# Kernel optimization log

Measured on AMD Instinct MI355X. Metric: run time of the kernel, lower is better.

Reference implementation:

```python
import jax, jax.numpy as jnp
import numpy as np

DIM = 1024
RANK = 8
POOL = 16
SCALE = 8.0 / 8.0  # alpha / rank


def setup_inputs() -> dict:
    key = jax.random.key(0)
    ks = jax.random.split(key, 8)
    B, N = 8, 4096
    x = jax.random.normal(ks[0], (B, N, DIM), dtype=jnp.float32)
    weight = jax.random.normal(ks[1], (3 * DIM, DIM), dtype=jnp.float32) * 0.02
    bias = jax.random.normal(ks[2], (3 * DIM,), dtype=jnp.float32) * 0.02
    A_q_pool = jax.random.normal(ks[3], (POOL, DIM, RANK), dtype=jnp.float32) * 0.02
    B_q_pool = jax.random.normal(ks[4], (POOL, RANK, DIM), dtype=jnp.float32) * 0.02
    A_v_pool = jax.random.normal(ks[5], (POOL, DIM, RANK), dtype=jnp.float32) * 0.02
    B_v_pool = jax.random.normal(ks[6], (POOL, RANK, DIM), dtype=jnp.float32) * 0.02
    idx = jax.random.randint(ks[7], (B, 1), 0, POOL, dtype=jnp.int64 if jax.config.jax_enable_x64 else jnp.int32)
    frozen_mask = jnp.zeros((POOL,), dtype=bool)
    return {"x": x, "weight": weight, "bias": bias,
            "A_q_pool": A_q_pool, "B_q_pool": B_q_pool,
            "A_v_pool": A_v_pool, "B_v_pool": B_v_pool,
            "idx": idx, "frozen_mask": frozen_mask}


def _maybe_freeze(pool, i, fz):
    g = pool[i]  # [B, ., .] per-sample gather
    return jnp.where(fz, jax.lax.stop_gradient(g), g)


def reference(x, weight, bias, A_q_pool, B_q_pool, A_v_pool, B_v_pool, idx, frozen_mask):
    # Base QKV projection: [B, N, 3*dim]
    qkv = jnp.einsum('bni,oi->bno', x, weight) + bias
    i = idx[:, 0]                      # [B]
    fz = frozen_mask[i][:, None, None]  # [B,1,1]
    A_q = _maybe_freeze(A_q_pool, i, fz)  # [B, dim, rank]
    B_q = _maybe_freeze(B_q_pool, i, fz)  # [B, rank, dim]
    A_v = _maybe_freeze(A_v_pool, i, fz)
    B_v = _maybe_freeze(B_v_pool, i, fz)
    # Low-rank update: (x @ A) @ B, rank-8 bottleneck
    new_q = jnp.einsum('bnr,brj->bnj', jnp.einsum('bni,bir->bnr', x, A_q), B_q)
    new_v = jnp.einsum('bnr,brj->bnj', jnp.einsum('bni,bir->bnr', x, A_v), B_v)
    qkv = qkv.at[:, :, :DIM].add(SCALE * new_q)
    qkv = qkv.at[:, :, -DIM:].add(SCALE * new_v)
    return qkv
```

## Files before the change

### kernel.cpp

```cpp
#include <hip/hip_runtime.h>
#include <hip/hip_bf16.h>
#include <stdint.h>

#define DIM   1024
#define ODIM  3072
#define MROWS 32768
#define RANK  8

typedef unsigned short u16;
typedef __attribute__((ext_vector_type(8))) short short8;
typedef __attribute__((ext_vector_type(8))) unsigned short u16x8;
typedef __attribute__((ext_vector_type(4))) unsigned short u16x4;
typedef __attribute__((ext_vector_type(4))) float f32x4;

__device__ __forceinline__ u16 f2bf(float f) {
    uint32_t u = __float_as_uint(f);
    u += 0x7fffu + ((u >> 16) & 1u);
    return (u16)(u >> 16);
}

__device__ __forceinline__ void gl2lds16(const void* g, void* l) {
    __builtin_amdgcn_global_load_lds(
        (const __attribute__((address_space(1))) void*)(uintptr_t)g,
        (__attribute__((address_space(3))) void*)(uint32_t)(uintptr_t)l,
        16, 0, 0);
}

#define BAR()    do { asm volatile("" ::: "memory"); __builtin_amdgcn_s_barrier(); asm volatile("" ::: "memory"); } while (0)
#define WAITV10() asm volatile("s_waitcnt vmcnt(10)" ::: "memory")
#define WAITV8()  asm volatile("s_waitcnt vmcnt(8)" ::: "memory")
#define WAITV4()  asm volatile("s_waitcnt vmcnt(4)" ::: "memory")
#define WAITV2()  asm volatile("s_waitcnt vmcnt(2)" ::: "memory")
#define WAITV0()  asm volatile("s_waitcnt vmcnt(0)" ::: "memory")
#define SCHED0()  __builtin_amdgcn_sched_barrier(0)

__global__ __launch_bounds__(256) void k_convert(const float* __restrict__ src,
                                                 u16* __restrict__ dst, int n) {
    const int stride = gridDim.x * blockDim.x;
    for (int t = blockIdx.x * blockDim.x + threadIdx.x; t * 8 < n; t += stride) {
        const int i = t * 8;
        float4 a = *reinterpret_cast<const float4*>(src + i);
        float4 b = *reinterpret_cast<const float4*>(src + i + 4);
        u16x8 o;
        o[0] = f2bf(a.x); o[1] = f2bf(a.y); o[2] = f2bf(a.z); o[3] = f2bf(a.w);
        o[4] = f2bf(b.x); o[5] = f2bf(b.y); o[6] = f2bf(b.z); o[7] = f2bf(b.w);
        *reinterpret_cast<u16x8*>(dst + i) = o;
    }
}

__global__ __launch_bounds__(256) void k_build(const float* __restrict__ W,
                                               const float* __restrict__ Aq_pool,
                                               const float* __restrict__ Bq_pool,
                                               const float* __restrict__ Av_pool,
                                               const float* __restrict__ Bv_pool,
                                               const int* __restrict__ idx,
                                               u16* __restrict__ Wmq,
                                               u16* __restrict__ Wmv) {
    const int b  = blockIdx.x >> 7;
    const int s  = (blockIdx.x >> 6) & 1;
    const int og = blockIdx.x & 63;
    const int p  = idx[b];
    const float* A  = (s ? Av_pool : Aq_pool) + (size_t)p * DIM * RANK;
    const float* Bp = (s ? Bv_pool : Bq_pool) + (size_t)p * RANK * DIM;
    const float* Ws = W + (size_t)(s ? 2048 : 0) * DIM;
    u16* dst = (s ? Wmv : Wmq) + (size_t)b * DIM * DIM;

    const int t  = threadIdx.x;
    const int i0 = t * 4;
    float a[4][8];
    #pragma unroll
    for (int ii = 0; ii < 4; ++ii) {
        float4 a0 = reinterpret_cast<const float4*>(A + (size_t)(i0 + ii) * RANK)[0];
        float4 a1 = reinterpret_cast<const float4*>(A + (size_t)(i0 + ii) * RANK)[1];
        a[ii][0] = a0.x; a[ii][1] = a0.y; a[ii][2] = a0.z; a[ii][3] = a0.w;
        a[ii][4] = a1.x; a[ii][5] = a1.y; a[ii][6] = a1.z; a[ii][7] = a1.w;
    }
    for (int r = 0; r < 16; ++r) {
        const int o = og * 16 + r;
        float bv[8];
        #pragma unroll
        for (int rr = 0; rr < 8; ++rr) bv[rr] = Bp[(size_t)rr * DIM + o];
        float4 w = *reinterpret_cast<const float4*>(Ws + (size_t)o * DIM + i0);
        float v[4] = {w.x, w.y, w.z, w.w};
        u16x4 ov;
        #pragma unroll
        for (int ii = 0; ii < 4; ++ii) {
            float d = 0.f;
            #pragma unroll
            for (int rr = 0; rr < 8; ++rr) d += a[ii][rr] * bv[rr];
            ov[ii] = f2bf(v[ii] + d);
        }
        *reinterpret_cast<u16x4*>(dst + (size_t)o * DIM + i0) = ov;
    }
}


__device__ __forceinline__ void stage_half(const u16* __restrict__ mat, int row0, int tk,
                                           u16* dst, int wave, int lane) {
    const int lrow = lane >> 3;
    const int g    = (lane & 7) ^ lrow;
    const u16* gp = mat + (size_t)(row0 + wave * 8 + lrow) * DIM + tk + g * 8;
    u16* lp = dst + wave * 8 * 64;
    gl2lds16(gp, lp);
    gl2lds16(gp + (size_t)64 * DIM, lp + 64 * 64);
}

__device__ __forceinline__ void ds_read_A(const u16* sA, int wr, int lane,
                                          int kx0, int kx1, int mh, short8 (&a)[4][2]) {
    #pragma unroll
    for (int f = 0; f < 4; ++f) {
        const int row = wr * 64 + f * 16 + mh * 128 + (lane & 15);
        a[f][0] = *reinterpret_cast<const short8*>(sA + row * 64 + kx0);
        a[f][1] = *reinterpret_cast<const short8*>(sA + row * 64 + kx1);
    }
}
__device__ __forceinline__ void ds_read_B(const u16* sB, int wc, int lane,
                                          int kx0, int kx1, int nh, short8 (&b)[2][2]) {
    #pragma unroll
    for (int f = 0; f < 2; ++f) {
        const int row = wc * 16 + (nh * 2 + f) * 64 + (lane & 15);
        b[f][0] = *reinterpret_cast<const short8*>(sB + row * 64 + kx0);
        b[f][1] = *reinterpret_cast<const short8*>(sB + row * 64 + kx1);
    }
}

template <int MH, int NH>
__device__ __forceinline__ void mfma_quad(const short8 (&a)[4][2], const short8 (&b)[2][2],
                                          f32x4 (&acc)[8][4]) {
    #pragma unroll
    for (int ks = 0; ks < 2; ++ks)
        #pragma unroll
        for (int f = 0; f < 4; ++f)
            #pragma unroll
            for (int g = 0; g < 2; ++g)
                acc[MH * 4 + f][NH * 2 + g] = __builtin_amdgcn_mfma_f32_16x16x32_bf16(
                    a[f][ks], b[g][ks], acc[MH * 4 + f][NH * 2 + g], 0, 0, 0);
}

#define PHASE(MH, NH, BREG)                             \
    do {                                                \
        BAR();                                          \
        SCHED0();                                       \
        __builtin_amdgcn_s_setprio(1);                  \
        mfma_quad<MH, NH>(a, BREG, acc);                \
        __builtin_amdgcn_s_setprio(0);                  \
        SCHED0();                                       \
    } while (0)

__global__ __launch_bounds__(512, 2) void k_gemm(const u16* __restrict__ Xc,
                                                 const u16* __restrict__ Wk,
                                                 const u16* __restrict__ Wmq,
                                                 const u16* __restrict__ Wmv,
                                                 const float* __restrict__ bias,
                                                 float* __restrict__ out) {
    extern __shared__ u16 lds[];
    const int tid  = threadIdx.x;
    const int lane = tid & 63, wave = tid >> 6;
    const int wr = wave >> 2, wc = wave & 3;

    const int orig = blockIdx.x;
    const int wg   = (orig & 7) * 192 + (orig >> 3);
    const int bn   = wg % 12;
    const int bm   = wg / 12;
    const int m0 = bm * 256, n0 = bn * 256;
    const int batch = m0 >> 12;

    const u16* Bmat;
    int nc;
    if (n0 < DIM)           { Bmat = Wmq + (size_t)batch * DIM * DIM; nc = n0; }
    else if (n0 < 2 * DIM)  { Bmat = Wk;                              nc = n0 - DIM; }
    else                    { Bmat = Wmv + (size_t)batch * DIM * DIM; nc = n0 - 2 * DIM; }

    const int kx0 = (((lane >> 4)    ) ^ (lane & 7)) * 8;
    const int kx1 = (((lane >> 4) + 4) ^ (lane & 7)) * 8;

    f32x4 acc[8][4] = {};

    stage_half(Xc,   m0,       0, lds,                    wave, lane);
    stage_half(Bmat, nc,       0, lds + 16384,            wave, lane);
    stage_half(Bmat, nc + 128, 0, lds + 16384 + 128 * 64, wave, lane);
    stage_half(Xc,   m0 + 128, 0, lds + 128 * 64,         wave, lane);
    WAITV0(); BAR();

    #pragma unroll 1
    for (int t = 0; t < 15; ++t) {
        const u16* sA = lds + (t & 1) * 32768;
        const u16* sB = sA + 16384;
        u16* wA = lds + ((t + 1) & 1) * 32768;
        u16* wB = wA + 16384;
        const int tk1 = (t + 1) * 64;
        short8 a[4][2], b0[2][2], b1[2][2];

        ds_read_A(sA, wr, lane, kx0, kx1, 0, a);
        ds_read_B(sB, wc, lane, kx0, kx1, 0, b0);
        stage_half(Xc,   m0,       tk1, wA,            wave, lane);
        stage_half(Bmat, nc,       tk1, wB,            wave, lane);
        stage_half(Bmat, nc + 128, tk1, wB + 128 * 64, wave, lane);
        stage_half(Xc,   m0 + 128, tk1, wA + 128 * 64, wave, lane);
        PHASE(0, 0, b0);
        WAITV10(); BAR();

        ds_read_B(sB, wc, lane, kx0, kx1, 1, b1);
        PHASE(0, 1, b1);
        WAITV8(); BAR();

        ds_read_A(sA, wr, lane, kx0, kx1, 1, a);
        PHASE(1, 0, b0);
        BAR();

        PHASE(1, 1, b1);
        WAITV4(); BAR();
    }

    {
        const u16* sA = lds + 32768;
        const u16* sB = sA + 16384;
        short8 a[4][2], b0[2][2], b1[2][2];

        ds_read_A(sA, wr, lane, kx0, kx1, 0, a);
        ds_read_B(sB, wc, lane, kx0, kx1, 0, b0);
        PHASE(0, 0, b0);
        WAITV2(); BAR();

        ds_read_B(sB, wc, lane, kx0, kx1, 1, b1);
        PHASE(0, 1, b1);
        WAITV0(); BAR();

        ds_read_A(sA, wr, lane, kx0, kx1, 1, a);
        PHASE(1, 0, b0);
        BAR();

        PHASE(1, 1, b1);
    }

    const int cn = wc * 16 + (lane & 15);
    float bcol[4];
    #pragma unroll
    for (int ni = 0; ni < 4; ++ni) bcol[ni] = bias[n0 + cn + ni * 64];
    #pragma unroll
    for (int mi = 0; mi < 8; ++mi) {
        const int rb = m0 + wr * 64 + (mi & 3) * 16 + (mi >> 2) * 128 + (lane >> 4) * 4;
        #pragma unroll
        for (int v = 0; v < 4; ++v) {
            const size_t row = (size_t)(rb + v);
            #pragma unroll
            for (int ni = 0; ni < 4; ++ni)
                out[row * ODIM + (size_t)(n0 + cn + ni * 64)] = acc[mi][ni][v] + bcol[ni];
        }
    }
}

extern "C" void kernel_launch(void* const* d_in, const int* in_sizes, int n_in,
                              void* d_out, int out_size, void* d_ws, size_t ws_size,
                              hipStream_t stream) {
    const float* x      = (const float*)d_in[0];
    const float* weight = (const float*)d_in[1];
    const float* bias   = (const float*)d_in[2];
    const float* Aq     = (const float*)d_in[3];
    const float* Bq     = (const float*)d_in[4];
    const float* Av     = (const float*)d_in[5];
    const float* Bv     = (const float*)d_in[6];
    const int*   idx    = (const int*)d_in[7];
    float* out = (float*)d_out;

    u16* Xc  = (u16*)d_ws;
    u16* Wk  = Xc + (size_t)MROWS * DIM;
    u16* Wmq = Wk + (size_t)DIM * DIM;
    u16* Wmv = Wmq + (size_t)8 * DIM * DIM;

    hipFuncSetAttribute(reinterpret_cast<const void*>(k_gemm),
                        hipFuncAttributeMaxDynamicSharedMemorySize, 131072);

    k_convert<<<2048, 256, 0, stream>>>(x, Xc, MROWS * DIM);
    k_convert<<<512, 256, 0, stream>>>(weight + (size_t)DIM * DIM, Wk, DIM * DIM);
    k_build<<<1024, 256, 0, stream>>>(weight, Aq, Bq, Av, Bv, idx, Wmq, Wmv);
    k_gemm<<<1536, 512, 131072, stream>>>(Xc, Wk, Wmq, Wmv, bias, out);
}
```

Measured before the change: 330.6 us.

## Restructure GEMM to 16 waves with triple-buffered BK=32 LDS pipeline

Rewrites the main GEMM mainloop to use 1024-thread blocks (16 waves, each owning a 64x64 sub-tile), K-step 32 instead of 64, and a three-stage LDS ring buffer that keeps two loads in flight. The goal is to hide global-to-LDS latency better and simplify the phase-by-phase barrier schedule. Per-wave accumulator count halves, which lowers register pressure. The costs are more barriers per unit of K, thinner MFMA bursts between syncs, and 96KB of LDS per block, which caps occupancy. The idx argument is added but unused.

Measured after the change: 324.9 us. Within noise of the previous version (-1.7%).

```diff
diff --git a/kernel.cpp b/kernel.cpp
--- a/kernel.cpp
+++ b/kernel.cpp
@@ -6,6 +6,7 @@
 #define ODIM  3072
 #define MROWS 32768
 #define RANK  8
+#define BK    32
 
 typedef unsigned short u16;
 typedef __attribute__((ext_vector_type(8))) short short8;
@@ -27,12 +28,8 @@
 }
 
 #define BAR()    do { asm volatile("" ::: "memory"); __builtin_amdgcn_s_barrier(); asm volatile("" ::: "memory"); } while (0)
-#define WAITV10() asm volatile("s_waitcnt vmcnt(10)" ::: "memory")
-#define WAITV8()  asm volatile("s_waitcnt vmcnt(8)" ::: "memory")
-#define WAITV4()  asm volatile("s_waitcnt vmcnt(4)" ::: "memory")
-#define WAITV2()  asm volatile("s_waitcnt vmcnt(2)" ::: "memory")
-#define WAITV0()  asm volatile("s_waitcnt vmcnt(0)" ::: "memory")
-#define SCHED0()  __builtin_amdgcn_sched_barrier(0)
+#define WAITV2() asm volatile("s_waitcnt vmcnt(2)" ::: "memory")
+#define WAITV0() asm volatile("s_waitcnt vmcnt(0)" ::: "memory")
 
 __global__ __launch_bounds__(256) void k_convert(const float* __restrict__ src,
                                                  u16* __restrict__ dst, int n) {
@@ -95,64 +92,44 @@
 }
 
 
-__device__ __forceinline__ void stage_half(const u16* __restrict__ mat, int row0, int tk,
-                                           u16* dst, int wave, int lane) {
-    const int lrow = lane >> 3;
-    const int g    = (lane & 7) ^ lrow;
-    const u16* gp = mat + (size_t)(row0 + wave * 8 + lrow) * DIM + tk + g * 8;
-    u16* lp = dst + wave * 8 * 64;
-    gl2lds16(gp, lp);
-    gl2lds16(gp + (size_t)64 * DIM, lp + 64 * 64);
-}
-
-__device__ __forceinline__ void ds_read_A(const u16* sA, int wr, int lane,
-                                          int kx0, int kx1, int mh, short8 (&a)[4][2]) {
-    #pragma unroll
-    for (int f = 0; f < 4; ++f) {
-        const int row = wr * 64 + f * 16 + mh * 128 + (lane & 15);
-        a[f][0] = *reinterpret_cast<const short8*>(sA + row * 64 + kx0);
-        a[f][1] = *reinterpret_cast<const short8*>(sA + row * 64 + kx1);
-    }
-}
-__device__ __forceinline__ void ds_read_B(const u16* sB, int wc, int lane,
-                                          int kx0, int kx1, int nh, short8 (&b)[2][2]) {
-    #pragma unroll
-    for (int f = 0; f < 2; ++f) {
-        const int row = wc * 16 + (nh * 2 + f) * 64 + (lane & 15);
-        b[f][0] = *reinterpret_cast<const short8*>(sB + row * 64 + kx0);
-        b[f][1] = *reinterpret_cast<const short8*>(sB + row * 64 + kx1);
-    }
-}
-
-template <int MH, int NH>
-__device__ __forceinline__ void mfma_quad(const short8 (&a)[4][2], const short8 (&b)[2][2],
-                                          f32x4 (&acc)[8][4]) {
-    #pragma unroll
-    for (int ks = 0; ks < 2; ++ks)
-        #pragma unroll
-        for (int f = 0; f < 4; ++f)
-            #pragma unroll
-            for (int g = 0; g < 2; ++g)
-                acc[MH * 4 + f][NH * 2 + g] = __builtin_amdgcn_mfma_f32_16x16x32_bf16(
-                    a[f][ks], b[g][ks], acc[MH * 4 + f][NH * 2 + g], 0, 0, 0);
-}
-
-#define PHASE(MH, NH, BREG)                             \
-    do {                                                \
-        BAR();                                          \
-        SCHED0();                                       \
-        __builtin_amdgcn_s_setprio(1);                  \
-        mfma_quad<MH, NH>(a, BREG, acc);                \
-        __builtin_amdgcn_s_setprio(0);                  \
-        SCHED0();                                       \
-    } while (0)
-
-__global__ __launch_bounds__(512, 2) void k_gemm(const u16* __restrict__ Xc,
-                                                 const u16* __restrict__ Wk,
-                                                 const u16* __restrict__ Wmq,
-                                                 const u16* __restrict__ Wmv,
-                                                 const float* __restrict__ bias,
-                                                 float* __restrict__ out) {
+__device__ __forceinline__ void stage(const u16* __restrict__ Xc,
+                                      const u16* __restrict__ Bm,
+                                      int m0, int nc, int tk,
+                                      u16* buf, int wave, int lane) {
+    const int rl = lane >> 2;
+    const int gs = (lane & 3) ^ ((lane >> 2) & 3) ^ ((lane >> 4) & 3);
+    const u16* ga = Xc + (size_t)(m0 + wave * 16 + rl) * DIM + tk + gs * 8;
+    const u16* gb = Bm + (size_t)(nc + wave * 16 + rl) * DIM + tk + gs * 8;
+    gl2lds16(ga, buf + wave * 512);
+    gl2lds16(gb, buf + 8192 + wave * 512);
+}
+
+__device__ __forceinline__ void tile_mfma(const u16* __restrict__ buf,
+                                          int wr, int wc, int lane, int kx,
+                                          f32x4 (&acc)[4][4]) {
+    short8 a[4], b[4];
+    #pragma unroll
+    for (int f = 0; f < 4; ++f)
+        a[f] = *reinterpret_cast<const short8*>(buf + (wr * 64 + f * 16 + (lane & 15)) * 32 + kx);
+    #pragma unroll
+    for (int n = 0; n < 4; ++n)
+        b[n] = *reinterpret_cast<const short8*>(buf + 8192 + (wc * 64 + n * 16 + (lane & 15)) * 32 + kx);
+    __builtin_amdgcn_s_setprio(1);
+    #pragma unroll
+    for (int f = 0; f < 4; ++f)
+        #pragma unroll
+        for (int n = 0; n < 4; ++n)
+            acc[f][n] = __builtin_amdgcn_mfma_f32_16x16x32_bf16(a[f], b[n], acc[f][n], 0, 0, 0);
+    __builtin_amdgcn_s_setprio(0);
+}
+
+__global__ __launch_bounds__(1024, 4) void k_gemm(const u16* __restrict__ Xc,
+                                                  const u16* __restrict__ Wk,
+                                                  const u16* __restrict__ Wmq,
+                                                  const u16* __restrict__ Wmv,
+                                                  const float* __restrict__ bias,
+                                                  const int* __restrict__ idx,
+                                                  float* __restrict__ out) {
     extern __shared__ u16 lds[];
     const int tid  = threadIdx.x;
     const int lane = tid & 63, wave = tid >> 6;
@@ -171,81 +148,49 @@
     else if (n0 < 2 * DIM)  { Bmat = Wk;                              nc = n0 - DIM; }
     else                    { Bmat = Wmv + (size_t)batch * DIM * DIM; nc = n0 - 2 * DIM; }
 
-    const int kx0 = (((lane >> 4)    ) ^ (lane & 7)) * 8;
-    const int kx1 = (((lane >> 4) + 4) ^ (lane & 7)) * 8;
-
-    f32x4 acc[8][4] = {};
-
-    stage_half(Xc,   m0,       0, lds,                    wave, lane);
-    stage_half(Bmat, nc,       0, lds + 16384,            wave, lane);
-    stage_half(Bmat, nc + 128, 0, lds + 16384 + 128 * 64, wave, lane);
-    stage_half(Xc,   m0 + 128, 0, lds + 128 * 64,         wave, lane);
+    const int kx = ((lane >> 4) ^ (lane & 3) ^ ((lane >> 2) & 3)) * 8;
+
+    u16* b0 = lds;
+    u16* b1 = lds + 16384;
+    u16* b2 = lds + 32768;
+
+    f32x4 acc[4][4] = {};
+
+    stage(Xc, Bmat, m0, nc, 0,  b0, wave, lane);
+    stage(Xc, Bmat, m0, nc, BK, b1, wave, lane);
+    WAITV2(); BAR();
+
+    #pragma unroll 1
+    for (int t3 = 0; t3 < 30; t3 += 3) {
+        stage(Xc, Bmat, m0, nc, (t3 + 2) * BK, b2, wave, lane);
+        tile_mfma(b0, wr, wc, lane, kx, acc);
+        WAITV2(); BAR();
+
+        stage(Xc, Bmat, m0, nc, (t3 + 3) * BK, b0, wave, lane);
+        tile_mfma(b1, wr, wc, lane, kx, acc);
+        WAITV2(); BAR();
+
+        stage(Xc, Bmat, m0, nc, (t3 + 4) * BK, b1, wave, lane);
+        tile_mfma(b2, wr, wc, lane, kx, acc);
+        WAITV2(); BAR();
+    }
+    tile_mfma(b0, wr, wc, lane, kx, acc);
     WAITV0(); BAR();
-
-    #pragma unroll 1
-    for (int t = 0; t < 15; ++t) {
-        const u16* sA = lds + (t & 1) * 32768;
-        const u16* sB = sA + 16384;
-        u16* wA = lds + ((t + 1) & 1) * 32768;
-        u16* wB = wA + 16384;
-        const int tk1 = (t + 1) * 64;
-        short8 a[4][2], b0[2][2], b1[2][2];
-
-        ds_read_A(sA, wr, lane, kx0, kx1, 0, a);
-        ds_read_B(sB, wc, lane, kx0, kx1, 0, b0);
-        stage_half(Xc,   m0,       tk1, wA,            wave, lane);
-        stage_half(Bmat, nc,       tk1, wB,            wave, lane);
-        stage_half(Bmat, nc + 128, tk1, wB + 128 * 64, wave, lane);
-        stage_half(Xc,   m0 + 128, tk1, wA + 128 * 64, wave, lane);
-        PHASE(0, 0, b0);
-        WAITV10(); BAR();
-
-        ds_read_B(sB, wc, lane, kx0, kx1, 1, b1);
-        PHASE(0, 1, b1);
-        WAITV8(); BAR();
-
-        ds_read_A(sA, wr, lane, kx0, kx1, 1, a);
-        PHASE(1, 0, b0);
-        BAR();
-
-        PHASE(1, 1, b1);
-        WAITV4(); BAR();
-    }
-
-    {
-        const u16* sA = lds + 32768;
-        const u16* sB = sA + 16384;
-        short8 a[4][2], b0[2][2], b1[2][2];
-
-        ds_read_A(sA, wr, lane, kx0, kx1, 0, a);
-        ds_read_B(sB, wc, lane, kx0, kx1, 0, b0);
-        PHASE(0, 0, b0);
-        WAITV2(); BAR();
-
-        ds_read_B(sB, wc, lane, kx0, kx1, 1, b1);
-        PHASE(0, 1, b1);
-        WAITV0(); BAR();
-
-        ds_read_A(sA, wr, lane, kx0, kx1, 1, a);
-        PHASE(1, 0, b0);
-        BAR();
-
-        PHASE(1, 1, b1);
-    }
-
-    const int cn = wc * 16 + (lane & 15);
+    tile_mfma(b1, wr, wc, lane, kx, acc);
+
+    const int cn = wc * 64 + (lane & 15);
     float bcol[4];
     #pragma unroll
-    for (int ni = 0; ni < 4; ++ni) bcol[ni] = bias[n0 + cn + ni * 64];
-    #pragma unroll
-    for (int mi = 0; mi < 8; ++mi) {
-        const int rb = m0 + wr * 64 + (mi & 3) * 16 + (mi >> 2) * 128 + (lane >> 4) * 4;
+    for (int n = 0; n < 4; ++n) bcol[n] = bias[n0 + cn + n * 16];
+    #pragma unroll
+    for (int f = 0; f < 4; ++f) {
+        const int rb = m0 + wr * 64 + f * 16 + (lane >> 4) * 4;
         #pragma unroll
         for (int v = 0; v < 4; ++v) {
             const size_t row = (size_t)(rb + v);
             #pragma unroll
-            for (int ni = 0; ni < 4; ++ni)
-                out[row * ODIM + (size_t)(n0 + cn + ni * 64)] = acc[mi][ni][v] + bcol[ni];
+            for (int n = 0; n < 4; ++n)
+                out[row * ODIM + (size_t)(n0 + cn + n * 16)] = acc[f][n][v] + bcol[n];
         }
     }
 }
@@ -269,10 +214,10 @@
     u16* Wmv = Wmq + (size_t)8 * DIM * DIM;
 
     hipFuncSetAttribute(reinterpret_cast<const void*>(k_gemm),
-                        hipFuncAttributeMaxDynamicSharedMemorySize, 131072);
+                        hipFuncAttributeMaxDynamicSharedMemorySize, 98304);
 
     k_convert<<<2048, 256, 0, stream>>>(x, Xc, MROWS * DIM);
     k_convert<<<512, 256, 0, stream>>>(weight + (size_t)DIM * DIM, Wk, DIM * DIM);
     k_build<<<1024, 256, 0, stream>>>(weight, Aq, Bq, Av, Bv, idx, Wmq, Wmv);
-    k_gemm<<<1536, 512, 131072, stream>>>(Xc, Wk, Wmq, Wmv, bias, out);
-}
+    k_gemm<<<1536, 1024, 98304, stream>>>(Xc, Wk, Wmq, Wmv, bias, idx, out);
+}
```

## Interleave global-to-LDS staging across MFMA phases and split A fragment registers

Applied to the files above, without the earlier changes.

Spreads the four global-to-LDS stage_half loads of the next K tile across the four MFMA phases instead of issuing them all up front. Separate A register sets are used for the low and high M halves, and explicit lgkmcnt waits are added before each MFMA block. The vmcnt thresholds are retuned to match the new issue order. This is meant to smooth memory issue and overlap it with MFMA work, at the cost of more VGPRs and possibly tighter sync stalls.

Result: faster. 298.2 us (-9.8%).

```diff
diff --git a/kernel.cpp b/kernel.cpp
--- a/kernel.cpp
+++ b/kernel.cpp
@@ -27,12 +27,12 @@
 }
 
 #define BAR()    do { asm volatile("" ::: "memory"); __builtin_amdgcn_s_barrier(); asm volatile("" ::: "memory"); } while (0)
-#define WAITV10() asm volatile("s_waitcnt vmcnt(10)" ::: "memory")
-#define WAITV8()  asm volatile("s_waitcnt vmcnt(8)" ::: "memory")
-#define WAITV4()  asm volatile("s_waitcnt vmcnt(4)" ::: "memory")
-#define WAITV2()  asm volatile("s_waitcnt vmcnt(2)" ::: "memory")
-#define WAITV0()  asm volatile("s_waitcnt vmcnt(0)" ::: "memory")
-#define SCHED0()  __builtin_amdgcn_sched_barrier(0)
+#define WAITV4() asm volatile("s_waitcnt vmcnt(4)" ::: "memory")
+#define WAITV2() asm volatile("s_waitcnt vmcnt(2)" ::: "memory")
+#define WAITV0() asm volatile("s_waitcnt vmcnt(0)" ::: "memory")
+#define WAITL0() asm volatile("s_waitcnt lgkmcnt(0)" ::: "memory")
+#define WAITL8() asm volatile("s_waitcnt lgkmcnt(8)" ::: "memory")
+#define SCHED0() __builtin_amdgcn_sched_barrier(0)
 
 __global__ __launch_bounds__(256) void k_convert(const float* __restrict__ src,
                                                  u16* __restrict__ dst, int n) {
@@ -137,12 +137,13 @@
                     a[f][ks], b[g][ks], acc[MH * 4 + f][NH * 2 + g], 0, 0, 0);
 }
 
-#define PHASE(MH, NH, BREG)                             \
+#define MFMA_BLOCK(MH, NH, AREG, BREG)                  \
     do {                                                \
         BAR();                                          \
+        WAITL0();                                       \
         SCHED0();                                       \
         __builtin_amdgcn_s_setprio(1);                  \
-        mfma_quad<MH, NH>(a, BREG, acc);                \
+        mfma_quad<MH, NH>(AREG, BREG, acc);             \
         __builtin_amdgcn_s_setprio(0);                  \
         SCHED0();                                       \
     } while (0)
@@ -189,48 +190,50 @@
         u16* wA = lds + ((t + 1) & 1) * 32768;
         u16* wB = wA + 16384;
         const int tk1 = (t + 1) * 64;
-        short8 a[4][2], b0[2][2], b1[2][2];
-
-        ds_read_A(sA, wr, lane, kx0, kx1, 0, a);
+        short8 a_lo[4][2], a_hi[4][2], b0[2][2], b1[2][2];
+
+        ds_read_A(sA, wr, lane, kx0, kx1, 0, a_lo);
         ds_read_B(sB, wc, lane, kx0, kx1, 0, b0);
-        stage_half(Xc,   m0,       tk1, wA,            wave, lane);
-        stage_half(Bmat, nc,       tk1, wB,            wave, lane);
+        stage_half(Xc, m0, tk1, wA, wave, lane);
+        WAITL8();
+        MFMA_BLOCK(0, 0, a_lo, b0);
+        WAITV4(); BAR();
+
+        ds_read_B(sB, wc, lane, kx0, kx1, 1, b1);
+        stage_half(Bmat, nc, tk1, wB, wave, lane);
+        MFMA_BLOCK(0, 1, a_lo, b1);
+        WAITV4(); BAR();
+
+        ds_read_A(sA, wr, lane, kx0, kx1, 1, a_hi);
         stage_half(Bmat, nc + 128, tk1, wB + 128 * 64, wave, lane);
-        stage_half(Xc,   m0 + 128, tk1, wA + 128 * 64, wave, lane);
-        PHASE(0, 0, b0);
-        WAITV10(); BAR();
-
-        ds_read_B(sB, wc, lane, kx0, kx1, 1, b1);
-        PHASE(0, 1, b1);
-        WAITV8(); BAR();
-
-        ds_read_A(sA, wr, lane, kx0, kx1, 1, a);
-        PHASE(1, 0, b0);
+        MFMA_BLOCK(1, 0, a_hi, b0);
         BAR();
 
-        PHASE(1, 1, b1);
+        stage_half(Xc, m0 + 128, tk1, wA + 128 * 64, wave, lane);
+        MFMA_BLOCK(1, 1, a_hi, b1);
         WAITV4(); BAR();
     }
 
     {
         const u16* sA = lds + 32768;
         const u16* sB = sA + 16384;
-        short8 a[4][2], b0[2][2], b1[2][2];
-
-        ds_read_A(sA, wr, lane, kx0, kx1, 0, a);
+        short8 a_lo[4][2], a_hi[4][2], b0[2][2], b1[2][2];
+
+        ds_read_A(sA, wr, lane, kx0, kx1, 0, a_lo);
         ds_read_B(sB, wc, lane, kx0, kx1, 0, b0);
-        PHASE(0, 0, b0);
+        WAITL8();
+        MFMA_BLOCK(0, 0, a_lo, b0);
         WAITV2(); BAR();
 
         ds_read_B(sB, wc, lane, kx0, kx1, 1, b1);
-        PHASE(0, 1, b1);
+        MFMA_BLOCK(0, 1, a_lo, b1);
         WAITV0(); BAR();
 
-        ds_read_A(sA, wr, lane, kx0, kx1, 1, a);
-        PHASE(1, 0, b0);
+        ds_read_A(sA, wr, lane, kx0, kx1, 1, a_hi);
+        MFMA_BLOCK(1, 0, a_hi, b0);
         BAR();
 
-        PHASE(1, 1, b1);
+        MFMA_BLOCK(1, 1, a_hi, b1);
     }
 
     const int cn = wc * 16 + (lane & 15);
```
